# Optimization experiments

Hardware: AMD Instinct MI355X
Metric: run time of the kernel (lower is better)

## Reference

```python
import jax, jax.numpy as jnp
import numpy as np

NUM_HEAD = 8
KEY_DIM = 256   # total key dim
VALUE_DIM = 256 # total value dim
OUT_DIM = 256
B, Q, K = 128, 384, 384


def setup_inputs() -> dict:
    key = jax.random.key(0)
    ks = jax.random.split(key, 11)
    hk = KEY_DIM // NUM_HEAD   # per-head key dim = 32
    hv = VALUE_DIM // NUM_HEAD # per-head value dim = 32
    s = 0.02
    return {
        "q_data": jax.random.normal(ks[0], (B, Q, KEY_DIM), jnp.float32),
        "m_data": jax.random.normal(ks[1], (B, K, VALUE_DIM), jnp.float32),
        "bias": jax.random.normal(ks[2], (B, 1, Q, K), jnp.float32),
        "nonbatched_bias": jax.random.normal(ks[3], (NUM_HEAD, Q, K), jnp.float32),
        "q_weights": jax.random.normal(ks[4], (KEY_DIM, NUM_HEAD, hk), jnp.float32) * s,
        "k_weights": jax.random.normal(ks[5], (VALUE_DIM, NUM_HEAD, hk), jnp.float32) * s,
        "v_weights": jax.random.normal(ks[6], (VALUE_DIM, NUM_HEAD, hv), jnp.float32) * s,
        "o_weights": jax.random.normal(ks[7], (NUM_HEAD, hv, OUT_DIM), jnp.float32) * s,
        "o_bias": jax.random.normal(ks[8], (OUT_DIM,), jnp.float32) * s,
        "gating_w": jax.random.normal(ks[9], (KEY_DIM, NUM_HEAD, hv), jnp.float32) * s,
        "gating_b": jnp.ones((NUM_HEAD, hv), jnp.float32),
    }


def reference(q_data, m_data, bias, nonbatched_bias,
              q_weights, k_weights, v_weights, o_weights, o_bias,
              gating_w, gating_b):
    hk = q_weights.shape[-1]
    scale = hk ** (-0.5)
    q = jnp.einsum('bqa,ahc->bqhc', q_data, q_weights) * scale
    k = jnp.einsum('bka,ahc->bkhc', m_data, k_weights)
    v = jnp.einsum('bka,ahc->bkhc', m_data, v_weights)
    # logits: [b,h,q,k] with additive pair bias and per-head nonbatched bias
    logits = jnp.einsum('bqhc,bkhc->bhqk', q, k) + bias + nonbatched_bias[None]
    weights = jax.nn.softmax(logits, axis=-1)
    weighted_avg = jnp.einsum('bhqk,bkhc->bqhc', weights, v)
    gate = jax.nn.sigmoid(jnp.einsum('bqc,chv->bqhv', q_data, gating_w) + gating_b)
    weighted_avg = weighted_avg * gate
    return jnp.einsum('bqhc,hco->bqo', weighted_avg, o_weights) + o_bias
```

## Files before the change

### kernel.cpp

```cpp
#include <hip/hip_runtime.h>
#include <hip/hip_bf16.h>

#define DM 256
#define NB 128
#define SQ 384
#define SK 384

typedef __bf16 bf16x4 __attribute__((ext_vector_type(4)));
typedef __bf16 bf16x8 __attribute__((ext_vector_type(8)));
typedef float f32x4 __attribute__((ext_vector_type(4)));
typedef unsigned short u16;
typedef unsigned int u32;

union BF8 { bf16x8 v8; bf16x4 v4[2]; uint2 u2[2]; };

__device__ __forceinline__ u16 f2bf(float f) {
    union { float fv; u32 u; } v; v.fv = f;
    u32 r = v.u + 0x7FFFu + ((v.u >> 16) & 1u);
    return (u16)(r >> 16);
}
__device__ __forceinline__ float bf2f(u16 u) {
    union { u32 v; float f; } x; x.v = ((u32)u) << 16; return x.f;
}
__device__ __forceinline__ uint2 pack4(float a, float b, float c, float d) {
    uint2 r;
    r.x = (u32)f2bf(a) | ((u32)f2bf(b) << 16);
    r.y = (u32)f2bf(c) | ((u32)f2bf(d) << 16);
    return r;
}
__device__ __forceinline__ uint2 pack4c(f32x4 v) {
    bf16x4 t;
    t[0] = (__bf16)v[0]; t[1] = (__bf16)v[1];
    t[2] = (__bf16)v[2]; t[3] = (__bf16)v[3];
    union { bf16x4 b; uint2 u; } cv; cv.b = t; return cv.u;
}
__device__ __forceinline__ void glds16(const void* g, void* l) {
    __builtin_amdgcn_global_load_lds(
        (const __attribute__((address_space(1))) unsigned int*)g,
        (__attribute__((address_space(3))) unsigned int*)l, 16, 0, 0);
}

__global__ __launch_bounds__(256)
void prep_w(const float* __restrict__ q_w, const float* __restrict__ k_w,
            const float* __restrict__ v_w, const float* __restrict__ g_w,
            const float* __restrict__ o_w, u16* __restrict__ wt)
{
    __shared__ float t[64][65];
    const int mat = blockIdx.z;
    const float* src = mat == 0 ? q_w : mat == 1 ? k_w : mat == 2 ? v_w : mat == 3 ? g_w : o_w;
    const float scale = (mat == 0) ? (float)(0.17677669529663687 * 1.4426950408889634) : 1.0f;
    const int k0 = blockIdx.x * 64, n0 = blockIdx.y * 64;
    const int tid = threadIdx.x;
#pragma unroll
    for (int i = 0; i < 4; ++i) {
        int pos = tid + i * 256;
        int r = pos >> 4, c4 = (pos & 15) * 4;
        f32x4 v = *(const f32x4*)&src[(size_t)(k0 + r) * DM + n0 + c4];
        t[r][c4 + 0] = v[0]; t[r][c4 + 1] = v[1]; t[r][c4 + 2] = v[2]; t[r][c4 + 3] = v[3];
    }
    __syncthreads();
    const int nr = tid >> 2, kq = (tid & 3) * 16;
    u16* dst = wt + (size_t)mat * DM * DM + (size_t)(n0 + nr) * DM + k0 + kq;
#pragma unroll
    for (int j = 0; j < 16; j += 4) {
        uint2 p = pack4(t[kq + j][nr] * scale, t[kq + j + 1][nr] * scale,
                        t[kq + j + 2][nr] * scale, t[kq + j + 3][nr] * scale);
        *(uint2*)&dst[j] = p;
    }
}

__global__ __launch_bounds__(256)
void prep_nb(const float* __restrict__ nb, float* __restrict__ nb2)
{
    int i = (blockIdx.x * 256 + threadIdx.x) * 4;
    f32x4 v = *(const f32x4*)&nb[i];
    *(f32x4*)&nb2[i] = v * 1.4426950408889634f - 20.0f;
}

template<int MODE>
__global__ __launch_bounds__(256)
void proj_kernel(const float* __restrict__ Af, const u16* __restrict__ Abf,
                 const u16* __restrict__ Wt1, const u16* __restrict__ Wt2,
                 const float* __restrict__ gb, const float* __restrict__ ob,
                 u16* __restrict__ out1, u16* __restrict__ gate,
                 u16* __restrict__ vT, float* __restrict__ outf)
{
    __shared__ u16 Wlds[64 * 256];
    const int tid = threadIdx.x, lane = tid & 63, w = tid >> 6;
    const int lr = lane & 15, lg = lane >> 4;
    const int m0 = blockIdx.x * 64;

    BF8 af[8];
    if (MODE <= 1) {
        const float* arow = Af + (size_t)(m0 + w * 16 + lr) * DM + 4 * lg;
#pragma unroll
        for (int ks = 0; ks < 8; ++ks) {
            f32x4 v0 = *(const f32x4*)&arow[ks * 32];
            f32x4 v1 = *(const f32x4*)&arow[ks * 32 + 16];
            af[ks].u2[0] = pack4(v0[0], v0[1], v0[2], v0[3]);
            af[ks].u2[1] = pack4(v1[0], v1[1], v1[2], v1[3]);
        }
    } else {
        const u16* arow = Abf + (size_t)(m0 + w * 16 + lr) * DM + 4 * lg;
#pragma unroll
        for (int ks = 0; ks < 8; ++ks) {
            af[ks].u2[0] = *(const uint2*)&arow[ks * 32];
            af[ks].u2[1] = *(const uint2*)&arow[ks * 32 + 16];
        }
    }

    const int NSLAB = (MODE == 2) ? 4 : 8;
    for (int sl = 0; sl < NSLAB; ++sl) {
        const u16* Wsrc = (sl < 4) ? Wt1 : Wt2;
        const int n0 = (sl & 3) * 64;
        if (sl) __syncthreads();
#pragma unroll
        for (int i = 0; i < 8; ++i) {
            int pos = tid + i * 256;
            int nr = pos >> 5, c8 = (pos & 31) * 8;
            uint4 gv = *(const uint4*)&Wsrc[(size_t)(n0 + nr) * DM + c8];
            int within = c8 & 31;
            int pa2 = (c8 >> 5) * 64 + ((within >> 3) & 1) * 32 + (within >> 4) * 8;
            int sw = (nr & 7) << 4;
            char* rb_ = (char*)Wlds + nr * 512;
            *(uint2*)(rb_ + (pa2 ^ sw)) = make_uint2(gv.x, gv.y);
            *(uint2*)(rb_ + ((pa2 + 16) ^ sw)) = make_uint2(gv.z, gv.w);
        }
        __syncthreads();

        f32x4 acc[4];
#pragma unroll
        for (int nf = 0; nf < 4; ++nf) acc[nf] = (f32x4){0.f, 0.f, 0.f, 0.f};
#pragma unroll
        for (int ks = 0; ks < 8; ++ks) {
#pragma unroll
            for (int nf = 0; nf < 4; ++nf) {
                int row = nf * 16 + lr;
                bf16x8 bfr = *(const bf16x8*)((char*)Wlds + row * 512 +
                                              ((ks * 64 + lg * 16) ^ ((row & 7) << 4)));
                acc[nf] = __builtin_amdgcn_mfma_f32_16x16x32_bf16(af[ks].v8, bfr, acc[nf], 0, 0, 0);
            }
        }

#pragma unroll
        for (int nf = 0; nf < 4; ++nf) {
            int n = n0 + nf * 16 + lr;
            int gn = (sl & 3) * 64 + nf * 16 + lr;
            if (MODE == 0) {
                if (sl < 4) {
#pragma unroll
                    for (int r = 0; r < 4; ++r)
                        out1[(size_t)(m0 + w * 16 + 4 * lg + r) * DM + n] = f2bf(acc[nf][r]);
                } else {
                    float gbv = gb[gn];
#pragma unroll
                    for (int r = 0; r < 4; ++r)
                        gate[(size_t)(m0 + w * 16 + 4 * lg + r) * DM + gn] =
                            f2bf(1.f / (1.f + __expf(-(acc[nf][r] + gbv))));
                }
            } else if (MODE == 1) {
                if (sl < 4) {
                    int pn = (n & ~31) | (((n >> 2) & 3) << 3) | (((n >> 4) & 1) << 2) | (n & 3);
#pragma unroll
                    for (int r = 0; r < 4; ++r)
                        out1[(size_t)(m0 + w * 16 + 4 * lg + r) * DM + pn] = f2bf(acc[nf][r]);
                } else {
                    int bb = m0 / SQ;
                    int kkl = m0 - bb * SQ + w * 16 + 4 * lg;
                    int cc = kkl & 31;
                    int kkp = (kkl & ~31) | (((cc >> 2) & 3) << 3) | (((cc >> 4) & 1) << 2);
                    *(uint2*)&vT[(size_t)(bb * DM + gn) * SK + kkp] =
                        pack4(acc[nf][0], acc[nf][1], acc[nf][2], acc[nf][3]);
                }
            } else {
                float obv = ob[n];
#pragma unroll
                for (int r = 0; r < 4; ++r)
                    outf[(size_t)(m0 + w * 16 + 4 * lg + r) * DM + n] = acc[nf][r] + obv;
            }
        }
    }
}

__global__ __launch_bounds__(512, 1)
void attn_kernel(const u16* __restrict__ Qb, const u16* __restrict__ Kb,
                 const u16* __restrict__ vT, const u16* __restrict__ gateb,
                 const float* __restrict__ bias, const float* __restrict__ nb2,
                 u16* __restrict__ wavg)
{
    extern __shared__ char smem[];
    const int tid = threadIdx.x, lane = tid & 63, h = tid >> 6;
    const int lr = lane & 15, lg = lane >> 4;
    const int bid = blockIdx.x;
    const int qt = bid >> 7, b = bid & 127;
    const int q0 = qt * 64;
    const float LOG2E = 1.4426950408889634f;

    const int ci0 = (h * 2) * 64 + lane, ci1 = (h * 2 + 1) * 64 + lane;
    const int kr0 = ci0 >> 5, kj0 = (ci0 & 31) ^ (kr0 & 7);
    const int kr1 = ci1 >> 5, kj1 = (ci1 & 31) ^ (kr1 & 7);
    const u16* kg0 = Kb + ((size_t)b * SK + kr0) * DM + kj0 * 8;
    const u16* kg1 = Kb + ((size_t)b * SK + kr1) * DM + kj1 * 8;
    const int vr0 = ci0 >> 2, vj0 = (ci0 & 3) ^ ((vr0 >> 1) & 3);
    const int vr1 = ci1 >> 2, vj1 = (ci1 & 3) ^ ((vr1 >> 1) & 3);
    const u16* vg0 = vT + ((size_t)b * DM + vr0) * SK + vj0 * 8;
    const u16* vg1 = vT + ((size_t)b * DM + vr1) * SK + vj1 * 8;
    const int cib = h * 64 + lane;
    const int bq = cib >> 3, bj = (cib & 7) ^ (bq & 7);
    const float* bg = bias + ((size_t)b * SQ + q0 + bq) * SK + bj * 4;

    const int kd0 = (h * 2) * 1024, kd1 = (h * 2 + 1) * 1024;
    const int bd = 32768 + h * 1024;

    BF8 qf[4];
    {
        const u16* qp = Qb + (size_t)(b * SQ + q0 + lr) * DM + h * 32 + 4 * lg;
#pragma unroll
        for (int nf = 0; nf < 4; ++nf) {
            qf[nf].u2[0] = *(const uint2*)&qp[nf * 16 * DM];
            qf[nf].u2[1] = *(const uint2*)&qp[nf * 16 * DM + 16];
        }
    }

    f32x4 Oacc[2][4];
    float lsum[4];
#pragma unroll
    for (int nf = 0; nf < 4; ++nf) {
        lsum[nf] = 0.f;
        Oacc[0][nf] = (f32x4){0.f, 0.f, 0.f, 0.f};
        Oacc[1][nf] = (f32x4){0.f, 0.f, 0.f, 0.f};
    }

    const float* np = nb2 + ((size_t)h * SQ + q0) * SK + 4 * lg;

    glds16(kg0, smem + kd0); glds16(kg1, smem + kd1);
    glds16(vg0, smem + 16384 + kd0); glds16(vg1, smem + 16384 + kd1);
    glds16(bg, smem + bd);
    kg0 += 32 * DM; kg1 += 32 * DM; vg0 += 32; vg1 += 32; bg += 32;
    asm volatile("s_waitcnt vmcnt(0)" ::: "memory");
    __syncthreads();

    int cur = 0;
#pragma unroll 1
    for (int kb = 0; kb < 12; ++kb) {
        const int k0 = kb * 32;
        if (kb < 11) {
            char* nbuf = smem + (cur ^ 1) * 40960;
            glds16(kg0, nbuf + kd0); glds16(kg1, nbuf + kd1);
            glds16(vg0, nbuf + 16384 + kd0); glds16(vg1, nbuf + 16384 + kd1);
            glds16(bg, nbuf + bd);
            kg0 += 32 * DM; kg1 += 32 * DM; vg0 += 32; vg1 += 32; bg += 32;
        }
        char* buf = smem + cur * 40960;
        char* Kc = buf; char* Vc = buf + 16384; char* Bc = buf + 32768;

        f32x4 st[4][2];
#pragma unroll
        for (int nf = 0; nf < 4; ++nf)
#pragma unroll
            for (int rb = 0; rb < 2; ++rb) {
                f32x4 n4 = *(const f32x4*)&np[(size_t)(nf * 16 + lr) * SK + k0 + rb * 16];
                f32x4 b4 = *(const f32x4*)(Bc + (nf * 16 + lr) * 128 +
                                           (((rb * 4 + lg) ^ (lr & 7)) << 4));
                f32x4 c4 = b4 * LOG2E + n4;
                bf16x8 kfr = *(const bf16x8*)(Kc + (rb * 16 + lr) * 512 +
                                              (((h * 4 + lg) ^ (lr & 7)) << 4));
                st[nf][rb] = __builtin_amdgcn_mfma_f32_16x16x32_bf16(kfr, qf[nf].v8, c4, 0, 0, 0);
            }

        BF8 pvv[4];
#pragma unroll
        for (int nf = 0; nf < 4; ++nf)
#pragma unroll
            for (int rb = 0; rb < 2; ++rb) {
                f32x4 e;
                e[0] = __builtin_amdgcn_exp2f(st[nf][rb][0]);
                e[1] = __builtin_amdgcn_exp2f(st[nf][rb][1]);
                e[2] = __builtin_amdgcn_exp2f(st[nf][rb][2]);
                e[3] = __builtin_amdgcn_exp2f(st[nf][rb][3]);
                lsum[nf] += (e[0] + e[1]) + (e[2] + e[3]);
                pvv[nf].u2[rb] = pack4c(e);
            }

#pragma unroll
        for (int cf = 0; cf < 2; ++cf) {
            int row = h * 32 + cf * 16 + lr;
            bf16x8 vfr = *(const bf16x8*)(Vc + row * 64 + ((lg ^ ((lr >> 1) & 3)) << 4));
#pragma unroll
            for (int nf = 0; nf < 4; ++nf)
                Oacc[cf][nf] = __builtin_amdgcn_mfma_f32_16x16x32_bf16(
                    vfr, pvv[nf].v8, Oacc[cf][nf], 0, 0, 0);
        }

        if (kb < 11) {
            asm volatile("s_waitcnt vmcnt(0)" ::: "memory");
            __syncthreads();
            cur ^= 1;
        }
    }

#pragma unroll
    for (int nf = 0; nf < 4; ++nf) {
        lsum[nf] += __shfl_xor(lsum[nf], 16, 64);
        lsum[nf] += __shfl_xor(lsum[nf], 32, 64);
    }

#pragma unroll
    for (int nf = 0; nf < 4; ++nf) {
        float rl = 1.0f / lsum[nf];
        size_t qrow = (size_t)(b * SQ + q0 + nf * 16 + lr);
#pragma unroll
        for (int cf = 0; cf < 2; ++cf) {
            size_t idx = qrow * DM + h * 32 + cf * 16 + 4 * lg;
            uint2 g2 = *(const uint2*)&gateb[idx];
            float g0 = bf2f((u16)(g2.x & 0xffff)), g1 = bf2f((u16)(g2.x >> 16));
            float g2f = bf2f((u16)(g2.y & 0xffff)), g3 = bf2f((u16)(g2.y >> 16));
            f32x4 o = Oacc[cf][nf];
            *(uint2*)&wavg[idx] = pack4(o[0] * rl * g0, o[1] * rl * g1,
                                        o[2] * rl * g2f, o[3] * rl * g3);
        }
    }
}

extern "C" void kernel_launch(void* const* d_in, const int* in_sizes, int n_in,
                              void* d_out, int out_size, void* d_ws, size_t ws_size,
                              hipStream_t stream) {
    const float* q_data = (const float*)d_in[0];
    const float* m_data = (const float*)d_in[1];
    const float* bias   = (const float*)d_in[2];
    const float* nbias  = (const float*)d_in[3];
    const float* q_w    = (const float*)d_in[4];
    const float* k_w    = (const float*)d_in[5];
    const float* v_w    = (const float*)d_in[6];
    const float* o_w    = (const float*)d_in[7];
    const float* o_b    = (const float*)d_in[8];
    const float* g_w    = (const float*)d_in[9];
    const float* g_b    = (const float*)d_in[10];
    float* out = (float*)d_out;

    const size_t MB = (size_t)NB * SQ * DM * 2;
    char* ws = (char*)d_ws;
    u16* qb    = (u16*)(ws);
    u16* kb    = (u16*)(ws + MB);
    u16* vTb   = (u16*)(ws + 2 * MB);
    u16* gateb = (u16*)(ws + 3 * MB);
    u16* wavg  = (u16*)(ws + 4 * MB);
    u16* wt    = (u16*)(ws + 5 * MB);
    float* nb2 = (float*)(ws + 5 * MB + 655360);
    u16* Wtq = wt, *Wtk = wt + 65536, *Wtv = wt + 2 * 65536,
       *Wtg = wt + 3 * 65536, *Wto = wt + 4 * 65536;

    prep_w<<<dim3(4, 4, 5), 256, 0, stream>>>(q_w, k_w, v_w, g_w, o_w, wt);
    prep_nb<<<1152, 256, 0, stream>>>(nbias, nb2);
    proj_kernel<0><<<768, 256, 0, stream>>>(q_data, nullptr, Wtq, Wtg, g_b, nullptr,
                                            qb, gateb, nullptr, nullptr);
    proj_kernel<1><<<768, 256, 0, stream>>>(m_data, nullptr, Wtk, Wtv, nullptr, nullptr,
                                            kb, nullptr, vTb, nullptr);

    const int ATTN_SMEM = 2 * 40960;
    hipFuncSetAttribute((const void*)attn_kernel,
                        hipFuncAttributeMaxDynamicSharedMemorySize, ATTN_SMEM);
    attn_kernel<<<768, 512, ATTN_SMEM, stream>>>(qb, kb, vTb, gateb, bias, nb2, wavg);

    proj_kernel<2><<<768, 256, 0, stream>>>(nullptr, wavg, Wto, nullptr, nullptr, o_b,
                                            nullptr, nullptr, nullptr, out);
}
```

Before: 282.9 us.

## Triple-buffer attention K/V/bias staging and hoist nonbatched-bias loads ahead of MFMAs

Moves the attention kernel's shared-memory staging from two buffers to three, so loads for block kb+2 are issued while block kb is computed. Each iteration now waits with a partial vmcnt instead of draining all outstanding loads. The nonbatched-bias global loads are issued up front, and the bias add moves out of the MFMA accumulator into the softmax step. MFMA sections are wrapped in s_setprio. In exchange, LDS per block grows from 80 KB to 120 KB, which may reduce occupancy, and the vmcnt counting depends on exactly how many loads are in flight.

```diff
diff --git a/kernel.cpp b/kernel.cpp
--- a/kernel.cpp
+++ b/kernel.cpp
@@ -233,55 +233,65 @@
 
     const float* np = nb2 + ((size_t)h * SQ + q0) * SK + 4 * lg;
 
-    glds16(kg0, smem + kd0); glds16(kg1, smem + kd1);
-    glds16(vg0, smem + 16384 + kd0); glds16(vg1, smem + 16384 + kd1);
-    glds16(bg, smem + bd);
-    kg0 += 32 * DM; kg1 += 32 * DM; vg0 += 32; vg1 += 32; bg += 32;
-    asm volatile("s_waitcnt vmcnt(0)" ::: "memory");
-    __syncthreads();
-
-    int cur = 0;
+    auto stage = [&](char* buf) {
+        glds16(kg0, buf + kd0); glds16(kg1, buf + kd1);
+        glds16(vg0, buf + 16384 + kd0); glds16(vg1, buf + 16384 + kd1);
+        glds16(bg, buf + bd);
+        kg0 += 32 * DM; kg1 += 32 * DM; vg0 += 32; vg1 += 32; bg += 32;
+    };
+
+    stage(smem);
+    stage(smem + 40960);
+    asm volatile("s_waitcnt vmcnt(5)" ::: "memory");
+    __builtin_amdgcn_s_barrier();
+
 #pragma unroll 1
     for (int kb = 0; kb < 12; ++kb) {
         const int k0 = kb * 32;
-        if (kb < 11) {
-            char* nbuf = smem + (cur ^ 1) * 40960;
-            glds16(kg0, nbuf + kd0); glds16(kg1, nbuf + kd1);
-            glds16(vg0, nbuf + 16384 + kd0); glds16(vg1, nbuf + 16384 + kd1);
-            glds16(bg, nbuf + bd);
-            kg0 += 32 * DM; kg1 += 32 * DM; vg0 += 32; vg1 += 32; bg += 32;
-        }
-        char* buf = smem + cur * 40960;
+        char* buf = smem + (kb % 3) * 40960;
         char* Kc = buf; char* Vc = buf + 16384; char* Bc = buf + 32768;
 
+        f32x4 n4r[4][2];
+#pragma unroll
+        for (int nf = 0; nf < 4; ++nf)
+#pragma unroll
+            for (int rb = 0; rb < 2; ++rb)
+                n4r[nf][rb] = *(const f32x4*)&np[(size_t)(nf * 16 + lr) * SK + k0 + rb * 16];
+        __builtin_amdgcn_sched_barrier(0);
+
+        if (kb < 10) stage(smem + ((kb + 2) % 3) * 40960);
+
         f32x4 st[4][2];
+        __builtin_amdgcn_s_setprio(1);
 #pragma unroll
         for (int nf = 0; nf < 4; ++nf)
 #pragma unroll
             for (int rb = 0; rb < 2; ++rb) {
-                f32x4 n4 = *(const f32x4*)&np[(size_t)(nf * 16 + lr) * SK + k0 + rb * 16];
+                bf16x8 kfr = *(const bf16x8*)(Kc + (rb * 16 + lr) * 512 +
+                                              (((h * 4 + lg) ^ (lr & 7)) << 4));
+                st[nf][rb] = __builtin_amdgcn_mfma_f32_16x16x32_bf16(
+                    kfr, qf[nf].v8, (f32x4){0.f, 0.f, 0.f, 0.f}, 0, 0, 0);
+            }
+        __builtin_amdgcn_s_setprio(0);
+
+        BF8 pvv[4];
+#pragma unroll
+        for (int nf = 0; nf < 4; ++nf)
+#pragma unroll
+            for (int rb = 0; rb < 2; ++rb) {
                 f32x4 b4 = *(const f32x4*)(Bc + (nf * 16 + lr) * 128 +
                                            (((rb * 4 + lg) ^ (lr & 7)) << 4));
-                f32x4 c4 = b4 * LOG2E + n4;
-                bf16x8 kfr = *(const bf16x8*)(Kc + (rb * 16 + lr) * 512 +
-                                              (((h * 4 + lg) ^ (lr & 7)) << 4));
-                st[nf][rb] = __builtin_amdgcn_mfma_f32_16x16x32_bf16(kfr, qf[nf].v8, c4, 0, 0, 0);
-            }
-
-        BF8 pvv[4];
-#pragma unroll
-        for (int nf = 0; nf < 4; ++nf)
-#pragma unroll
-            for (int rb = 0; rb < 2; ++rb) {
+                f32x4 s = st[nf][rb] + b4 * LOG2E + n4r[nf][rb];
                 f32x4 e;
-                e[0] = __builtin_amdgcn_exp2f(st[nf][rb][0]);
-                e[1] = __builtin_amdgcn_exp2f(st[nf][rb][1]);
-                e[2] = __builtin_amdgcn_exp2f(st[nf][rb][2]);
-                e[3] = __builtin_amdgcn_exp2f(st[nf][rb][3]);
+                e[0] = __builtin_amdgcn_exp2f(s[0]);
+                e[1] = __builtin_amdgcn_exp2f(s[1]);
+                e[2] = __builtin_amdgcn_exp2f(s[2]);
+                e[3] = __builtin_amdgcn_exp2f(s[3]);
                 lsum[nf] += (e[0] + e[1]) + (e[2] + e[3]);
                 pvv[nf].u2[rb] = pack4c(e);
             }
 
+        __builtin_amdgcn_s_setprio(1);
 #pragma unroll
         for (int cf = 0; cf < 2; ++cf) {
             int row = h * 32 + cf * 16 + lr;
@@ -291,12 +301,11 @@
                 Oacc[cf][nf] = __builtin_amdgcn_mfma_f32_16x16x32_bf16(
                     vfr, pvv[nf].v8, Oacc[cf][nf], 0, 0, 0);
         }
-
-        if (kb < 11) {
-            asm volatile("s_waitcnt vmcnt(0)" ::: "memory");
-            __syncthreads();
-            cur ^= 1;
-        }
+        __builtin_amdgcn_s_setprio(0);
+
+        if (kb < 10)      asm volatile("s_waitcnt vmcnt(5)" ::: "memory");
+        else if (kb == 10) asm volatile("s_waitcnt vmcnt(0)" ::: "memory");
+        if (kb < 11) __builtin_amdgcn_s_barrier();
     }
 
 #pragma unroll
@@ -357,7 +366,7 @@
     proj_kernel<1><<<768, 256, 0, stream>>>(m_data, nullptr, Wtk, Wtv, nullptr, nullptr,
                                             kb, nullptr, vTb, nullptr);
 
-    const int ATTN_SMEM = 2 * 40960;
+    const int ATTN_SMEM = 3 * 40960;
     hipFuncSetAttribute((const void*)attn_kernel,
                         hipFuncAttributeMaxDynamicSharedMemorySize, ATTN_SMEM);
     attn_kernel<<<768, 512, ATTN_SMEM, stream>>>(qb, kb, vTb, gateb, bias, nb2, wavg);
```

Measured after the change: 284.8 us. No clear change (+0.7%).
